# Kernel tuning notes

Measured on AMD Instinct MI355X. Metric: run time of the kernel, lower is better.

Reference implementation:

```python
import jax, jax.numpy as jnp
import numpy as np

EPS = 1e-5

def silu(x):
    return x * jax.nn.sigmoid(x)

def layernorm(x, g, b):
    m = jnp.mean(x, axis=-1, keepdims=True)
    v = jnp.var(x, axis=-1, keepdims=True)
    return (x - m) * jax.lax.rsqrt(v + EPS) * g + b

def mamba(x, in_w, conv_w, conv_b, xproj_w, dt_w, dt_b, A_log, Dp, out_w):
    # x: (B, L, d_model)
    B_, L, _ = x.shape
    d_inner, d_conv = conv_w.shape
    d_state = A_log.shape[1]
    dt_rank = dt_w.shape[1]
    xz = x @ in_w.T                     # (B, L, 2*d_inner)
    u, z = jnp.split(xz, 2, axis=-1)
    # causal depthwise conv1d, kernel size d_conv, truncated to L
    up = jnp.pad(u, ((0, 0), (d_conv - 1, 0), (0, 0))).transpose(0, 2, 1)  # (B, C, L+K-1)
    uc = jax.lax.conv_general_dilated(up, conv_w[:, None, :], (1,), 'VALID',
                                      feature_group_count=d_inner)        # (B, C, L)
    u = silu(uc.transpose(0, 2, 1) + conv_b)                               # (B, L, d_inner)
    dbc = u @ xproj_w.T                                                    # (B, L, dt_rank+2*d_state)
    dt, Bm, Cm = jnp.split(dbc, [dt_rank, dt_rank + d_state], axis=-1)
    delta = jax.nn.softplus(dt @ dt_w.T + dt_b)                            # (B, L, d_inner)
    A = -jnp.exp(A_log)                                                    # (d_inner, d_state)
    dA = jnp.exp(delta[..., None] * A)                                     # (B, L, d_inner, d_state)
    dBu = delta[..., None] * Bm[:, :, None, :] * u[..., None]

    def step(h, inp):
        dA_t, dBu_t, C_t = inp
        h = dA_t * h + dBu_t                                               # (B, d_inner, d_state)
        y = jnp.einsum('bdn,bn->bd', h, C_t)
        return h, y

    h0 = jnp.zeros((B_, d_inner, d_state), x.dtype)
    _, ys = jax.lax.scan(step, h0, (dA.transpose(1, 0, 2, 3),
                                    dBu.transpose(1, 0, 2, 3),
                                    Cm.transpose(1, 0, 2)))
    y = ys.transpose(1, 0, 2) + u * Dp
    y = y * silu(z)
    return y @ out_w.T

def decoder_layer(x,
                  f_in_w, f_conv_w, f_conv_b, f_xproj_w, f_dt_w, f_dt_b, f_A_log, f_D, f_out_w,
                  r_in_w, r_conv_w, r_conv_b, r_xproj_w, r_dt_w, r_dt_b, r_A_log, r_D, r_out_w,
                  conv1_w, conv1_b, conv2_w, conv2_b, ln1_g, ln1_b, ln2_g, ln2_b):
    fwd = mamba(x, f_in_w, f_conv_w, f_conv_b, f_xproj_w, f_dt_w, f_dt_b, f_A_log, f_D, f_out_w)
    bwd = jnp.flip(mamba(jnp.flip(x, axis=1), r_in_w, r_conv_w, r_conv_b, r_xproj_w,
                         r_dt_w, r_dt_b, r_A_log, r_D, r_out_w), axis=1)
    x1 = layernorm(x + fwd + bwd, ln1_g, ln1_b)
    # kernel-size-1 Conv1d == pointwise linear; dropout is identity at eval
    y = jax.nn.gelu(x1 @ conv1_w.T + conv1_b, approximate=False)
    y = y @ conv2_w.T + conv2_b
    return layernorm(x1 + y, ln2_g, ln2_b)

def setup_inputs() -> dict:
    key = jax.random.key(0)
    ks = jax.random.split(key, 32)
    d_model, d_state, d_inner, dt_rank, d_ff = 512, 16, 1024, 32, 2048
    B, L = 8, 512
    s = 0.02
    inp = {}
    inp['x'] = jax.random.normal(ks[0], (B, L, d_model), jnp.float32)
    i = 1
    for p in ('f', 'r'):
        inp[p + '_in_w'] = jax.random.normal(ks[i], (2 * d_inner, d_model)) * s; i += 1
        inp[p + '_conv_w'] = jax.random.normal(ks[i], (d_inner, 4)) * 0.2; i += 1
        inp[p + '_conv_b'] = jax.random.normal(ks[i], (d_inner,)) * s; i += 1
        inp[p + '_xproj_w'] = jax.random.normal(ks[i], (dt_rank + 2 * d_state, d_inner)) * s; i += 1
        inp[p + '_dt_w'] = jax.random.normal(ks[i], (d_inner, dt_rank)) * s; i += 1
        inp[p + '_dt_b'] = jax.random.normal(ks[i], (d_inner,)) * s; i += 1
        inp[p + '_A_log'] = jax.random.uniform(ks[i], (d_inner, d_state)); i += 1
        inp[p + '_D'] = jax.random.normal(ks[i], (d_inner,)) * s + 1.0; i += 1
        inp[p + '_out_w'] = jax.random.normal(ks[i], (d_model, d_inner)) * s; i += 1
    inp['conv1_w'] = jax.random.normal(ks[i], (d_ff, d_model)) * s; i += 1
    inp['conv1_b'] = jax.random.normal(ks[i], (d_ff,)) * s; i += 1
    inp['conv2_w'] = jax.random.normal(ks[i], (d_model, d_ff)) * s; i += 1
    inp['conv2_b'] = jax.random.normal(ks[i], (d_model,)) * s; i += 1
    inp['ln1_g'] = jnp.ones((d_model,)); inp['ln1_b'] = jnp.zeros((d_model,))
    inp['ln2_g'] = jnp.ones((d_model,)); inp['ln2_b'] = jnp.zeros((d_model,))
    return inp

def reference(x,
              f_in_w, f_conv_w, f_conv_b, f_xproj_w, f_dt_w, f_dt_b, f_A_log, f_D, f_out_w,
              r_in_w, r_conv_w, r_conv_b, r_xproj_w, r_dt_w, r_dt_b, r_A_log, r_D, r_out_w,
              conv1_w, conv1_b, conv2_w, conv2_b, ln1_g, ln1_b, ln2_g, ln2_b):
    return decoder_layer(x,
                         f_in_w, f_conv_w, f_conv_b, f_xproj_w, f_dt_w, f_dt_b, f_A_log, f_D, f_out_w,
                         r_in_w, r_conv_w, r_conv_b, r_xproj_w, r_dt_w, r_dt_b, r_A_log, r_D, r_out_w,
                         conv1_w, conv1_b, conv2_w, conv2_b, ln1_g, ln1_b, ln2_g, ln2_b)
```

## Files before the change

kernel.cpp:

```cpp
#include <hip/hip_runtime.h>
#include <hip/hip_bf16.h>

#define DEVINL __device__ __forceinline__

typedef short bf16x8 __attribute__((ext_vector_type(8)));
typedef float f32x4 __attribute__((ext_vector_type(4)));
typedef ushort ushort8v __attribute__((ext_vector_type(8)));

static constexpr int Bn = 8, Ln = 512, DM = 512, DI = 1024, DS = 16, DFF = 2048;
static constexpr int Mtok = Bn * Ln;
static constexpr int NCH = 32, CLS = 16;

DEVINL float bf2f(ushort u) { union { uint i; float f; } v; v.i = uint(u) << 16; return v.f; }
DEVINL ushort f2bf(float f) {
  union { float f; uint i; } v; v.f = f;
  uint r = v.i + 0x7FFF + ((v.i >> 16) & 1);
  return ushort(r >> 16);
}

#define GLOAD16(gp, lp)                                                        \
  __builtin_amdgcn_global_load_lds(                                            \
      (const __attribute__((address_space(1))) void*)(gp),                     \
      (__attribute__((address_space(3))) void*)(lp), 16, 0, 0)

struct CvtJob { const float* src; ushort* dst; int blk0; int _pad; };
struct CvtTab { CvtJob j[11]; };

__global__ __launch_bounds__(256)
void cvt_k(CvtTab tb, int njobs) {
  const int blk = blockIdx.x;
  int ji = 0;
#pragma unroll
  for (int k = 1; k < 11; ++k)
    if (k < njobs && tb.j[k].blk0 <= blk) ji = k;
  const CvtJob J = tb.j[ji];
  const size_t base = (size_t)(blk - J.blk0) * 2048 + (size_t)threadIdx.x * 8;
  float4 a = *(const float4*)(J.src + base);
  float4 b = *(const float4*)(J.src + base + 4);
  ushort8v o;
  o[0] = f2bf(a.x); o[1] = f2bf(a.y); o[2] = f2bf(a.z); o[3] = f2bf(a.w);
  o[4] = f2bf(b.x); o[5] = f2bf(b.y); o[6] = f2bf(b.z); o[7] = f2bf(b.w);
  *(ushort8v*)(J.dst + base) = o;
}

template<int BM, int BN, int WM, int WN, int EPI, int OUTF32, int DUALK>
__global__ __launch_bounds__(256)
void gemm_lds(const ushort* __restrict__ A0, const ushort* __restrict__ W0,
              void* __restrict__ C0v, const float* __restrict__ bias0,
              const ushort* __restrict__ A1, const ushort* __restrict__ W1,
              void* __restrict__ C1v, const float* __restrict__ bias1,
              const ushort* __restrict__ Ab0, const ushort* __restrict__ Wb0,
              int K, int lda, int ldw, int ldc, int Kb, int ldab, int ldwb)
{
  constexpr int MT = BM / WM / 16, NT = BN / WN / 16;
  constexpr int RA = BM * 32 / 2048, RB = BN * 32 / 2048;
  __shared__ ushort As[BM * 32];
  __shared__ ushort Bs[BN * 32];

  const ushort* Ap = blockIdx.z ? A1 : A0;
  const ushort* Wp = blockIdx.z ? W1 : W0;
  void* Cv         = blockIdx.z ? C1v : C0v;
  const float* bia = blockIdx.z ? bias1 : bias0;

  const int tid = threadIdx.x, lane = tid & 63, wv = tid >> 6;
  const int wm = wv / WN, wn = wv % WN;
  const int mbase = blockIdx.x * BM, nbase = blockIdx.y * BN;
  const int r = lane & 15, ko = (lane >> 4) * 8;

  f32x4 acc[MT][NT];
#pragma unroll
  for (int mi = 0; mi < MT; ++mi)
#pragma unroll
    for (int ni = 0; ni < NT; ++ni) acc[mi][ni] = (f32x4){0.f, 0.f, 0.f, 0.f};

  for (int blkK = 0; blkK < (DUALK ? 2 : 1); ++blkK) {
    const ushort* Au = (DUALK && blkK) ? Ab0 : Ap;
    const ushort* Wu = (DUALK && blkK) ? Wb0 : Wp;
    const int Ku  = (DUALK && blkK) ? Kb : K;
    const int ldau = (DUALK && blkK) ? ldab : lda;
    const int ldwu = (DUALK && blkK) ? ldwb : ldw;

    for (int k0 = 0; k0 < Ku; k0 += 32) {
      __syncthreads();
#pragma unroll
      for (int i = 0; i < RA; ++i) {
        const int e = i * 2048 + wv * 512 + lane * 8;
        const int row = e >> 5, ck = e & 31;
        GLOAD16(Au + (size_t)(mbase + row) * ldau + k0 + ck,
                (ushort*)As + i * 2048 + wv * 512);
      }
#pragma unroll
      for (int i = 0; i < RB; ++i) {
        const int e = i * 2048 + wv * 512 + lane * 8;
        const int row = e >> 5, ck = e & 31;
        GLOAD16(Wu + (size_t)(nbase + row) * ldwu + k0 + ck,
                (ushort*)Bs + i * 2048 + wv * 512);
      }
      __syncthreads();

      bf16x8 af[MT], bfv[NT];
#pragma unroll
      for (int mi = 0; mi < MT; ++mi)
        af[mi] = *(const bf16x8*)&As[(wm * MT * 16 + mi * 16 + r) * 32 + ko];
#pragma unroll
      for (int ni = 0; ni < NT; ++ni)
        bfv[ni] = *(const bf16x8*)&Bs[(wn * NT * 16 + ni * 16 + r) * 32 + ko];
#pragma unroll
      for (int mi = 0; mi < MT; ++mi)
#pragma unroll
        for (int ni = 0; ni < NT; ++ni)
          acc[mi][ni] = __builtin_amdgcn_mfma_f32_16x16x32_bf16(af[mi], bfv[ni], acc[mi][ni], 0, 0, 0);
    }
  }

  const int rr = (lane >> 4) * 4, cc = lane & 15;
#pragma unroll
  for (int ni = 0; ni < NT; ++ni) {
    const int col = nbase + wn * NT * 16 + ni * 16 + cc;
    float bsv = 0.f;
    if (EPI >= 1) bsv = bia[col];
#pragma unroll
    for (int mi = 0; mi < MT; ++mi) {
#pragma unroll
      for (int j = 0; j < 4; ++j) {
        const int row = mbase + wm * MT * 16 + mi * 16 + rr + j;
        float v = acc[mi][ni][j] + bsv;
        if (EPI == 2) v = (v > 20.f) ? v : __logf(1.f + __expf(v));
        if (EPI == 3) v = 0.5f * v * (1.f + erff(v * 0.70710678f));
        if (OUTF32) ((float*)Cv)[(size_t)row * ldc + col] = v;
        else        ((ushort*)Cv)[(size_t)row * ldc + col] = f2bf(v);
      }
    }
  }
}

template<int WAVES_M, int WAVES_N, int MT, int NT, int EPI, int OUTF32>
__global__ __launch_bounds__(WAVES_M * WAVES_N * 64)
void gemm_k(const ushort* __restrict__ A0, const ushort* __restrict__ W0,
            void* __restrict__ C0v, const float* __restrict__ bias0,
            const ushort* __restrict__ A1, const ushort* __restrict__ W1,
            void* __restrict__ C1v, const float* __restrict__ bias1,
            int K, int lda, int ldw, int ldc)
{
  const ushort* A   = blockIdx.z ? A1 : A0;
  const ushort* W   = blockIdx.z ? W1 : W0;
  void* Cv          = blockIdx.z ? C1v : C0v;
  const float* bia  = blockIdx.z ? bias1 : bias0;

  const int tid = threadIdx.x, lane = tid & 63, wv = tid >> 6;
  const int wm = wv / WAVES_N, wn = wv % WAVES_N;
  const int r = lane & 15, ko = (lane >> 4) * 8;
  const int mbase = blockIdx.x * (WAVES_M * MT * 16) + wm * (MT * 16);
  const int nbase = blockIdx.y * (WAVES_N * NT * 16) + wn * (NT * 16);

  f32x4 acc[MT][NT];
#pragma unroll
  for (int mi = 0; mi < MT; ++mi)
#pragma unroll
    for (int ni = 0; ni < NT; ++ni) acc[mi][ni] = (f32x4){0.f, 0.f, 0.f, 0.f};

  const ushort* arow[MT];
  const ushort* wrow[NT];
#pragma unroll
  for (int mi = 0; mi < MT; ++mi) arow[mi] = A + (size_t)(mbase + mi * 16 + r) * lda + ko;
#pragma unroll
  for (int ni = 0; ni < NT; ++ni) wrow[ni] = W + (size_t)(nbase + ni * 16 + r) * ldw + ko;
  for (int k0 = 0; k0 < K; k0 += 32) {
    bf16x8 av[MT], bv[NT];
#pragma unroll
    for (int mi = 0; mi < MT; ++mi) av[mi] = *(const bf16x8*)(arow[mi] + k0);
#pragma unroll
    for (int ni = 0; ni < NT; ++ni) bv[ni] = *(const bf16x8*)(wrow[ni] + k0);
#pragma unroll
    for (int mi = 0; mi < MT; ++mi)
#pragma unroll
      for (int ni = 0; ni < NT; ++ni)
        acc[mi][ni] = __builtin_amdgcn_mfma_f32_16x16x32_bf16(av[mi], bv[ni], acc[mi][ni], 0, 0, 0);
  }

  const int rr = (lane >> 4) * 4, cc = lane & 15;
#pragma unroll
  for (int ni = 0; ni < NT; ++ni) {
    const int col = nbase + ni * 16 + cc;
    float bsv = 0.f;
    if (EPI >= 1) bsv = bia[col];
#pragma unroll
    for (int mi = 0; mi < MT; ++mi) {
#pragma unroll
      for (int j = 0; j < 4; ++j) {
        const int row = mbase + mi * 16 + rr + j;
        float v = acc[mi][ni][j] + bsv;
        if (EPI == 2) v = (v > 20.f) ? v : __logf(1.f + __expf(v));
        if (OUTF32) ((float*)Cv)[(size_t)row * ldc + col] = v;
        else        ((ushort*)Cv)[(size_t)row * ldc + col] = f2bf(v);
      }
    }
  }
}

__global__ __launch_bounds__(256)
void xproj_k(const ushort* __restrict__ A0, const ushort* __restrict__ W0,
             ushort* __restrict__ C0,
             const ushort* __restrict__ A1, const ushort* __restrict__ W1,
             ushort* __restrict__ C1)
{
  const ushort* A = blockIdx.z ? A1 : A0;
  const ushort* W = blockIdx.z ? W1 : W0;
  ushort* C       = blockIdx.z ? C1 : C0;

  const int tid = threadIdx.x, lane = tid & 63, wv = tid >> 6;
  const int r = lane & 15, ko = (lane >> 4) * 8;
  const int mbase = blockIdx.x * 16;
  const int nbase = wv * 16;

  f32x4 acc = (f32x4){0.f, 0.f, 0.f, 0.f};
  const ushort* ap = A + (size_t)(mbase + r) * DI + ko;
  const ushort* wp = W + (size_t)(nbase + r) * DI + ko;
#pragma unroll 4
  for (int k0 = 0; k0 < DI; k0 += 32) {
    const bf16x8 av = *(const bf16x8*)(ap + k0);
    const bf16x8 bv = *(const bf16x8*)(wp + k0);
    acc = __builtin_amdgcn_mfma_f32_16x16x32_bf16(av, bv, acc, 0, 0, 0);
  }
  const int cc = lane & 15, rr = (lane >> 4) * 4;
#pragma unroll
  for (int j = 0; j < 4; ++j)
    C[(size_t)(mbase + rr + j) * 64 + nbase + cc] = f2bf(acc[j]);
}

__global__ __launch_bounds__(256)
void conv_k(const ushort* __restrict__ xz_f, const ushort* __restrict__ xz_r,
            const float* __restrict__ fw, const float* __restrict__ fb,
            const float* __restrict__ rw, const float* __restrict__ rb,
            ushort* __restrict__ u_f, ushort* __restrict__ u_r,
            ushort* __restrict__ gz_f, ushort* __restrict__ gz_r)
{
  int idx = blockIdx.x * 256 + threadIdx.x;
  int dir = idx >> 19;
  int rem = idx & ((1 << 19) - 1);
  int bt = rem >> 7;
  int c0 = (rem & 127) * 8;
  int b = bt >> 9, t = bt & 511;
  const ushort* xz = dir ? xz_r : xz_f;
  const float* cw = dir ? rw : fw;
  const float* cb = dir ? rb : fb;
  ushort* uo = dir ? u_r : u_f;
  ushort* go = dir ? gz_r : gz_f;

  float acc[8];
#pragma unroll
  for (int j = 0; j < 8; ++j) acc[j] = cb[c0 + j];
  float wgt[8][4];
#pragma unroll
  for (int j = 0; j < 8; ++j) {
    float4 w4 = *(const float4*)(cw + (size_t)(c0 + j) * 4);
    wgt[j][0] = w4.x; wgt[j][1] = w4.y; wgt[j][2] = w4.z; wgt[j][3] = w4.w;
  }
#pragma unroll
  for (int k = 0; k < 4; ++k) {
    int tt = dir ? (t + 3 - k) : (t - 3 + k);
    if (tt < 0 || tt >= Ln) continue;
    ushort8v v = *(const ushort8v*)(xz + ((size_t)(b * Ln + tt) * 2048 + c0));
#pragma unroll
    for (int j = 0; j < 8; ++j) acc[j] += wgt[j][k] * bf2f(v[j]);
  }
  ushort8v outv;
#pragma unroll
  for (int j = 0; j < 8; ++j) {
    float s = acc[j];
    outv[j] = f2bf(s / (1.f + __expf(-s)));
  }
  *(ushort8v*)(uo + (size_t)bt * DI + c0) = outv;

  ushort8v zv = *(const ushort8v*)(xz + ((size_t)bt * 2048 + DI + c0));
  ushort8v gv;
#pragma unroll
  for (int j = 0; j < 8; ++j) {
    float z = bf2f(zv[j]);
    gv[j] = f2bf(z / (1.f + __expf(-z)));
  }
  *(ushort8v*)(go + (size_t)bt * DI + c0) = gv;
}

__global__ __launch_bounds__(256, 4)
void scan1_k(const ushort* __restrict__ delta_f, const ushort* __restrict__ delta_r,
             const ushort* __restrict__ u_f, const ushort* __restrict__ u_r,
             const ushort* __restrict__ dbc_f, const ushort* __restrict__ dbc_r,
             const float* __restrict__ fA, const float* __restrict__ rA,
             float4* __restrict__ hloc, float* __restrict__ Sa)
{
  const int bid = blockIdx.x;
  const int part = bid & 3, chunk = (bid >> 2) & 31, b = (bid >> 7) & 7, dir = bid >> 10;
  const int tid = threadIdx.x, c = part * 256 + tid;

  const ushort* dl_p = dir ? delta_r : delta_f;
  const ushort* u_p  = dir ? u_r : u_f;
  const ushort* dbc  = dir ? dbc_r : dbc_f;
  const float*  Alog = dir ? rA : fA;

  __shared__ float Bs[CLS][16];
  {
    const int s = tid >> 4, n = tid & 15;
    const int t = dir ? (Ln - 1 - (chunk * CLS + s)) : (chunk * CLS + s);
    Bs[s][n] = bf2f(dbc[(size_t)(b * Ln + t) * 64 + 32 + n]);
  }
  __syncthreads();

  float a2[16];
  {
    const float4* Ar = (const float4*)(Alog + (size_t)c * 16);
#pragma unroll
    for (int g = 0; g < 4; ++g) {
      float4 av = Ar[g];
      a2[g*4+0] = -__expf(av.x) * 1.44269504f;
      a2[g*4+1] = -__expf(av.y) * 1.44269504f;
      a2[g*4+2] = -__expf(av.z) * 1.44269504f;
      a2[g*4+3] = -__expf(av.w) * 1.44269504f;
    }
  }

  const int t0 = dir ? (Ln - 1 - chunk * CLS) : (chunk * CLS);
  const int stp = (dir ? -1 : 1) * DI;
  const ushort* dlp = dl_p + (size_t)(b * Ln + t0) * DI + c;
  const ushort* up  = u_p  + (size_t)(b * Ln + t0) * DI + c;

  float h[16];
#pragma unroll
  for (int n = 0; n < 16; ++n) h[n] = 0.f;
  float S = 0.f;

#pragma unroll 2
  for (int s = 0; s < CLS; ++s) {
    const float dl = bf2f(*dlp); dlp += stp;
    const float uv = bf2f(*up); up += stp;
    const float du = dl * uv;
    S += dl;
#pragma unroll
    for (int g = 0; g < 4; ++g) {
      const float4 Bv = ((const float4*)Bs[s])[g];
      h[g*4+0] = fmaf(exp2f(dl * a2[g*4+0]), h[g*4+0], du * Bv.x);
      h[g*4+1] = fmaf(exp2f(dl * a2[g*4+1]), h[g*4+1], du * Bv.y);
      h[g*4+2] = fmaf(exp2f(dl * a2[g*4+2]), h[g*4+2], du * Bv.z);
      h[g*4+3] = fmaf(exp2f(dl * a2[g*4+3]), h[g*4+3], du * Bv.w);
    }
  }
  const size_t o = ((size_t)((dir * 8 + b) * NCH + chunk) * 1024 + c);
#pragma unroll
  for (int g = 0; g < 4; ++g)
    hloc[o * 4 + g] = (float4){h[g*4+0], h[g*4+1], h[g*4+2], h[g*4+3]};
  Sa[o] = S;
}

__global__ __launch_bounds__(256, 4)
void scan2_k(float4* __restrict__ hloc, const float* __restrict__ Sa,
             const float* __restrict__ fA, const float* __restrict__ rA)
{
  const int idx = blockIdx.x * 256 + threadIdx.x;
  const int ng = idx & 3, c = (idx >> 2) & 1023, b = (idx >> 12) & 7, dir = idx >> 15;
  const float* Alog = dir ? rA : fA;
  float a2[4];
  {
    const float4 av = *(const float4*)(Alog + (size_t)c * 16 + ng * 4);
    a2[0] = -__expf(av.x) * 1.44269504f;
    a2[1] = -__expf(av.y) * 1.44269504f;
    a2[2] = -__expf(av.z) * 1.44269504f;
    a2[3] = -__expf(av.w) * 1.44269504f;
  }
  float4 h = (float4){0.f, 0.f, 0.f, 0.f};
  const size_t base = (size_t)(dir * 8 + b) * NCH * 1024 + c;
#pragma unroll
  for (int k = 0; k < NCH; ++k) {
    const size_t o = base + (size_t)k * 1024;
    const float S = Sa[o];
    const float4 hl = hloc[o * 4 + ng];
    hloc[o * 4 + ng] = h;
    h.x = fmaf(exp2f(a2[0] * S), h.x, hl.x);
    h.y = fmaf(exp2f(a2[1] * S), h.y, hl.y);
    h.z = fmaf(exp2f(a2[2] * S), h.z, hl.z);
    h.w = fmaf(exp2f(a2[3] * S), h.w, hl.w);
  }
}

__global__ __launch_bounds__(256, 4)
void scan3_k(const ushort* __restrict__ delta_f, const ushort* __restrict__ delta_r,
             const ushort* __restrict__ u_f, const ushort* __restrict__ u_r,
             const ushort* __restrict__ dbc_f, const ushort* __restrict__ dbc_r,
             const ushort* __restrict__ gz_f, const ushort* __restrict__ gz_r,
             const float* __restrict__ fA, const float* __restrict__ fD,
             const float* __restrict__ rA, const float* __restrict__ rD,
             const float4* __restrict__ hin,
             ushort* __restrict__ ym_f, ushort* __restrict__ ym_r)
{
  const int bid = blockIdx.x;
  const int part = bid & 3, chunk = (bid >> 2) & 31, b = (bid >> 7) & 7, dir = bid >> 10;
  const int tid = threadIdx.x, c = part * 256 + tid;

  const ushort* dl_p = dir ? delta_r : delta_f;
  const ushort* u_p  = dir ? u_r : u_f;
  const ushort* dbc  = dir ? dbc_r : dbc_f;
  const ushort* gz   = dir ? gz_r : gz_f;
  const float*  Alog = dir ? rA : fA;
  const float*  Dw   = dir ? rD : fD;
  ushort* ym         = dir ? ym_r : ym_f;

  __shared__ float Bs[CLS][16], Cs[CLS][16];
  {
    const int s = tid >> 5, k = tid & 31;
#pragma unroll
    for (int p = 0; p < 2; ++p) {
      const int ss = s + p * 8;
      const int t = dir ? (Ln - 1 - (chunk * CLS + ss)) : (chunk * CLS + ss);
      const float val = bf2f(dbc[(size_t)(b * Ln + t) * 64 + 32 + k]);
      if (k < 16) Bs[ss][k] = val; else Cs[ss][k - 16] = val;
    }
  }
  __syncthreads();

  float a2[16];
  {
    const float4* Ar = (const float4*)(Alog + (size_t)c * 16);
#pragma unroll
    for (int g = 0; g < 4; ++g) {
      float4 av = Ar[g];
      a2[g*4+0] = -__expf(av.x) * 1.44269504f;
      a2[g*4+1] = -__expf(av.y) * 1.44269504f;
      a2[g*4+2] = -__expf(av.z) * 1.44269504f;
      a2[g*4+3] = -__expf(av.w) * 1.44269504f;
    }
  }
  const float Dc = Dw[c];

  float h[16];
  {
    const size_t o = ((size_t)((dir * 8 + b) * NCH + chunk) * 1024 + c) * 4;
#pragma unroll
    for (int g = 0; g < 4; ++g) {
      const float4 hv = hin[o + g];
      h[g*4+0] = hv.x; h[g*4+1] = hv.y; h[g*4+2] = hv.z; h[g*4+3] = hv.w;
    }
  }

  const int t0 = dir ? (Ln - 1 - chunk * CLS) : (chunk * CLS);
  const int stp = (dir ? -1 : 1) * DI;
  const ushort* dlp = dl_p + (size_t)(b * Ln + t0) * DI + c;
  const ushort* up  = u_p  + (size_t)(b * Ln + t0) * DI + c;
  const ushort* gp  = gz   + (size_t)(b * Ln + t0) * DI + c;
  ushort*       ymp = ym   + (size_t)(b * Ln + t0) * DI + c;

#pragma unroll 2
  for (int s = 0; s < CLS; ++s) {
    const float dl = bf2f(*dlp); dlp += stp;
    const float uv = bf2f(*up); up += stp;
    const float gg = bf2f(*gp); gp += stp;
    const float du = dl * uv;
    float y = 0.f;
#pragma unroll
    for (int g = 0; g < 4; ++g) {
      const float4 Bv = ((const float4*)Bs[s])[g];
      const float4 Cw = ((const float4*)Cs[s])[g];
      h[g*4+0] = fmaf(exp2f(dl * a2[g*4+0]), h[g*4+0], du * Bv.x); y = fmaf(h[g*4+0], Cw.x, y);
      h[g*4+1] = fmaf(exp2f(dl * a2[g*4+1]), h[g*4+1], du * Bv.y); y = fmaf(h[g*4+1], Cw.y, y);
      h[g*4+2] = fmaf(exp2f(dl * a2[g*4+2]), h[g*4+2], du * Bv.z); y = fmaf(h[g*4+2], Cw.z, y);
      h[g*4+3] = fmaf(exp2f(dl * a2[g*4+3]), h[g*4+3], du * Bv.w); y = fmaf(h[g*4+3], Cw.w, y);
    }
    *ymp = f2bf((y + uv * Dc) * gg); ymp += stp;
  }
}

template<int OUTF32>
__global__ __launch_bounds__(256)
void ln_k(const ushort* __restrict__ a, const ushort* __restrict__ b,
          const float* __restrict__ g, const float* __restrict__ bb,
          void* __restrict__ outv)
{
  const int row = blockIdx.x, tid = threadIdx.x;
  const size_t base = (size_t)row * DM;
  float v0 = bf2f(a[base + tid]) + bf2f(b[base + tid]);
  float v1 = bf2f(a[base + tid + 256]) + bf2f(b[base + tid + 256]);
  float s1 = v0 + v1, s2 = v0 * v0 + v1 * v1;
  for (int o = 32; o; o >>= 1) { s1 += __shfl_down(s1, o); s2 += __shfl_down(s2, o); }
  __shared__ float l1[4], l2[4];
  const int wv = tid >> 6, ln = tid & 63;
  if (ln == 0) { l1[wv] = s1; l2[wv] = s2; }
  __syncthreads();
  const float t1 = l1[0] + l1[1] + l1[2] + l1[3];
  const float t2 = l2[0] + l2[1] + l2[2] + l2[3];
  const float mean = t1 * (1.f / 512.f);
  const float var = t2 * (1.f / 512.f) - mean * mean;
  const float rs = rsqrtf(var + 1e-5f);
  const float o0 = (v0 - mean) * rs * g[tid] + bb[tid];
  const float o1 = (v1 - mean) * rs * g[tid + 256] + bb[tid + 256];
  if (OUTF32) {
    ((float*)outv)[base + tid] = o0;
    ((float*)outv)[base + tid + 256] = o1;
  } else {
    ((ushort*)outv)[base + tid] = f2bf(o0);
    ((ushort*)outv)[base + tid + 256] = f2bf(o1);
  }
}

extern "C" void kernel_launch(void* const* d_in, const int* in_sizes, int n_in,
                              void* d_out, int out_size, void* d_ws, size_t ws_size,
                              hipStream_t stream)
{
  const float* x        = (const float*)d_in[0];
  const float* f_in_w   = (const float*)d_in[1];
  const float* f_conv_w = (const float*)d_in[2];
  const float* f_conv_b = (const float*)d_in[3];
  const float* f_xproj  = (const float*)d_in[4];
  const float* f_dt_w   = (const float*)d_in[5];
  const float* f_dt_b   = (const float*)d_in[6];
  const float* f_A_log  = (const float*)d_in[7];
  const float* f_D      = (const float*)d_in[8];
  const float* f_out_w  = (const float*)d_in[9];
  const float* r_in_w   = (const float*)d_in[10];
  const float* r_conv_w = (const float*)d_in[11];
  const float* r_conv_b = (const float*)d_in[12];
  const float* r_xproj  = (const float*)d_in[13];
  const float* r_dt_w   = (const float*)d_in[14];
  const float* r_dt_b   = (const float*)d_in[15];
  const float* r_A_log  = (const float*)d_in[16];
  const float* r_D      = (const float*)d_in[17];
  const float* r_out_w  = (const float*)d_in[18];
  const float* conv1_w  = (const float*)d_in[19];
  const float* conv1_b  = (const float*)d_in[20];
  const float* conv2_w  = (const float*)d_in[21];
  const float* conv2_b  = (const float*)d_in[22];
  const float* ln1_g    = (const float*)d_in[23];
  const float* ln1_b    = (const float*)d_in[24];
  const float* ln2_g    = (const float*)d_in[25];
  const float* ln2_b    = (const float*)d_in[26];

  char* ws = (char*)d_ws;
  size_t off = 0;
  auto alloc = [&](size_t bytes) -> void* {
    void* p = ws + off;
    off += (bytes + 255) & ~(size_t)255;
    return p;
  };
  ushort* x_b     = (ushort*)alloc((size_t)Mtok * DM * 2);
  ushort* f_inw_b = (ushort*)alloc((size_t)2 * DI * DM * 2);
  ushort* r_inw_b = (ushort*)alloc((size_t)2 * DI * DM * 2);
  ushort* f_xp_b  = (ushort*)alloc((size_t)64 * DI * 2);
  ushort* r_xp_b  = (ushort*)alloc((size_t)64 * DI * 2);
  ushort* f_dtw_b = (ushort*)alloc((size_t)DI * 32 * 2);
  ushort* r_dtw_b = (ushort*)alloc((size_t)DI * 32 * 2);
  ushort* f_ow_b  = (ushort*)alloc((size_t)DM * DI * 2);
  ushort* r_ow_b  = (ushort*)alloc((size_t)DM * DI * 2);
  ushort* c1w_b   = (ushort*)alloc((size_t)DFF * DM * 2);
  ushort* c2w_b   = (ushort*)alloc((size_t)DM * DFF * 2);
  ushort* xz_f    = (ushort*)alloc((size_t)Mtok * 2048 * 2);
  ushort* xz_r    = (ushort*)alloc((size_t)Mtok * 2048 * 2);
  ushort* u_f     = (ushort*)alloc((size_t)Mtok * DI * 2);
  ushort* u_r     = (ushort*)alloc((size_t)Mtok * DI * 2);
  ushort* gz_f    = (ushort*)alloc((size_t)Mtok * DI * 2);
  ushort* gz_r    = (ushort*)alloc((size_t)Mtok * DI * 2);
  ushort* dbc_f   = (ushort*)alloc((size_t)Mtok * 64 * 2);
  ushort* dbc_r   = (ushort*)alloc((size_t)Mtok * 64 * 2);
  ushort* delta_f = (ushort*)alloc((size_t)Mtok * DI * 2);
  ushort* delta_r = (ushort*)alloc((size_t)Mtok * DI * 2);
  ushort* ym_f    = (ushort*)alloc((size_t)Mtok * DI * 2);
  ushort* ym_r    = (ushort*)alloc((size_t)Mtok * DI * 2);
  ushort* mo      = (ushort*)alloc((size_t)Mtok * DM * 2);
  ushort* x1      = (ushort*)alloc((size_t)Mtok * DM * 2);
  ushort* h1b     = (ushort*)alloc((size_t)Mtok * DFF * 2);
  ushort* y2      = (ushort*)alloc((size_t)Mtok * DM * 2);
  float4* hloc    = (float4*)alloc((size_t)2 * 8 * NCH * 1024 * 4 * 16);
  float*  Sa      = (float*)alloc((size_t)2 * 8 * NCH * 1024 * 4);
  (void)ws_size; (void)in_sizes; (void)n_in; (void)out_size;

  {
    CvtTab tb;
    int blk = 0, ji = 0;
    auto add = [&](const float* s, ushort* d, int n) {
      tb.j[ji].src = s; tb.j[ji].dst = d; tb.j[ji].blk0 = blk; tb.j[ji]._pad = 0;
      blk += n / 2048; ++ji;
    };
    add(x,       x_b,     Mtok * DM);
    add(f_in_w,  f_inw_b, 2 * DI * DM);
    add(r_in_w,  r_inw_b, 2 * DI * DM);
    add(f_xproj, f_xp_b,  64 * DI);
    add(r_xproj, r_xp_b,  64 * DI);
    add(f_dt_w,  f_dtw_b, DI * 32);
    add(r_dt_w,  r_dtw_b, DI * 32);
    add(f_out_w, f_ow_b,  DM * DI);
    add(r_out_w, r_ow_b,  DM * DI);
    add(conv1_w, c1w_b,   DFF * DM);
    add(conv2_w, c2w_b,   DM * DFF);
    cvt_k<<<dim3(blk), 256, 0, stream>>>(tb, ji);
  }

  gemm_lds<128, 128, 2, 2, 0, 0, 0><<<dim3(32, 16, 2), 256, 0, stream>>>(
      x_b, f_inw_b, xz_f, nullptr, x_b, r_inw_b, xz_r, nullptr,
      nullptr, nullptr, DM, DM, DM, 2048, 0, 0, 0);

  conv_k<<<dim3(2 * Mtok * DI / 8 / 256), 256, 0, stream>>>(
      xz_f, xz_r, f_conv_w, f_conv_b, r_conv_w, r_conv_b, u_f, u_r, gz_f, gz_r);

  xproj_k<<<dim3(256, 1, 2), 256, 0, stream>>>(
      u_f, f_xp_b, dbc_f, u_r, r_xp_b, dbc_r);

  gemm_k<4, 1, 1, 4, 2, 0><<<dim3(64, 16, 2), 256, 0, stream>>>(
      dbc_f, f_dtw_b, delta_f, f_dt_b, dbc_r, r_dtw_b, delta_r, r_dt_b,
      32, 64, 32, DI);

  scan1_k<<<dim3(2048), 256, 0, stream>>>(
      delta_f, delta_r, u_f, u_r, dbc_f, dbc_r, f_A_log, r_A_log, hloc, Sa);
  scan2_k<<<dim3(256), 256, 0, stream>>>(hloc, Sa, f_A_log, r_A_log);
  scan3_k<<<dim3(2048), 256, 0, stream>>>(
      delta_f, delta_r, u_f, u_r, dbc_f, dbc_r, gz_f, gz_r,
      f_A_log, f_D, r_A_log, r_D, hloc, ym_f, ym_r);

  gemm_lds<64, 64, 2, 2, 0, 0, 1><<<dim3(64, 8, 1), 256, 0, stream>>>(
      ym_f, f_ow_b, mo, nullptr, nullptr, nullptr, nullptr, nullptr,
      ym_r, r_ow_b, DI, DI, DI, DM, DI, DI, DI);

  ln_k<0><<<dim3(Mtok), 256, 0, stream>>>(x_b, mo, ln1_g, ln1_b, x1);

  gemm_lds<128, 128, 2, 2, 3, 0, 0><<<dim3(32, 16, 1), 256, 0, stream>>>(
      x1, c1w_b, h1b, conv1_b, nullptr, nullptr, nullptr, nullptr,
      nullptr, nullptr, DM, DM, DM, DFF, 0, 0, 0);

  gemm_lds<64, 64, 2, 2, 1, 0, 0><<<dim3(64, 8, 1), 256, 0, stream>>>(
      h1b, c2w_b, y2, conv2_b, nullptr, nullptr, nullptr, nullptr,
      nullptr, nullptr, DFF, DFF, DFF, DM, 0, 0, 0);

  ln_k<1><<<dim3(Mtok), 256, 0, stream>>>(x1, y2, ln2_g, ln2_b, (float*)d_out);
}
```

Before: 278.8 us.

## Split SSM state across thread pairs in scan kernels and relayout hloc

Each channel's 16-state recurrence is now handled by two adjacent threads with 8 states each, doubling the block count for scan1 and scan3. The y partial sums are combined with a lane shuffle and only one lane writes the output. The hloc buffer is relaid out as state-group-major so scan1, scan2 and scan3 access it with coalesced float4 loads and stores. The aim is more parallelism and lower register pressure in the chunked scan, at the cost of duplicated delta/u/gate loads per channel and a shuffle per timestep.

```diff
diff --git a/kernel.cpp b/kernel.cpp
--- a/kernel.cpp
+++ b/kernel.cpp
@@ -290,8 +290,9 @@
              float4* __restrict__ hloc, float* __restrict__ Sa)
 {
   const int bid = blockIdx.x;
-  const int part = bid & 3, chunk = (bid >> 2) & 31, b = (bid >> 7) & 7, dir = bid >> 10;
-  const int tid = threadIdx.x, c = part * 256 + tid;
+  const int part = bid & 7, chunk = (bid >> 3) & 31, b = (bid >> 8) & 7, dir = bid >> 11;
+  const int tid = threadIdx.x, half = tid & 1, c = part * 128 + (tid >> 1);
+  const int bd = dir * 8 + b;
 
   const ushort* dl_p = dir ? delta_r : delta_f;
   const ushort* u_p  = dir ? u_r : u_f;
@@ -306,11 +307,11 @@
   }
   __syncthreads();
 
-  float a2[16];
+  float a2[8];
   {
-    const float4* Ar = (const float4*)(Alog + (size_t)c * 16);
-#pragma unroll
-    for (int g = 0; g < 4; ++g) {
+    const float4* Ar = (const float4*)(Alog + (size_t)c * 16 + half * 8);
+#pragma unroll
+    for (int g = 0; g < 2; ++g) {
       float4 av = Ar[g];
       a2[g*4+0] = -__expf(av.x) * 1.44269504f;
       a2[g*4+1] = -__expf(av.y) * 1.44269504f;
@@ -324,9 +325,9 @@
   const ushort* dlp = dl_p + (size_t)(b * Ln + t0) * DI + c;
   const ushort* up  = u_p  + (size_t)(b * Ln + t0) * DI + c;
 
-  float h[16];
-#pragma unroll
-  for (int n = 0; n < 16; ++n) h[n] = 0.f;
+  float h[8];
+#pragma unroll
+  for (int n = 0; n < 8; ++n) h[n] = 0.f;
   float S = 0.f;
 
 #pragma unroll 2
@@ -336,19 +337,21 @@
     const float du = dl * uv;
     S += dl;
 #pragma unroll
-    for (int g = 0; g < 4; ++g) {
-      const float4 Bv = ((const float4*)Bs[s])[g];
+    for (int g = 0; g < 2; ++g) {
+      const float4 Bv = ((const float4*)Bs[s])[half * 2 + g];
       h[g*4+0] = fmaf(exp2f(dl * a2[g*4+0]), h[g*4+0], du * Bv.x);
       h[g*4+1] = fmaf(exp2f(dl * a2[g*4+1]), h[g*4+1], du * Bv.y);
       h[g*4+2] = fmaf(exp2f(dl * a2[g*4+2]), h[g*4+2], du * Bv.z);
       h[g*4+3] = fmaf(exp2f(dl * a2[g*4+3]), h[g*4+3], du * Bv.w);
     }
   }
-  const size_t o = ((size_t)((dir * 8 + b) * NCH + chunk) * 1024 + c);
-#pragma unroll
-  for (int g = 0; g < 4; ++g)
-    hloc[o * 4 + g] = (float4){h[g*4+0], h[g*4+1], h[g*4+2], h[g*4+3]};
-  Sa[o] = S;
+#pragma unroll
+  for (int g = 0; g < 2; ++g) {
+    const size_t o = ((size_t)(half * 2 + g) * 16 * NCH + (size_t)bd * NCH + chunk) * 1024 + c;
+    hloc[o] = (float4){h[g*4+0], h[g*4+1], h[g*4+2], h[g*4+3]};
+  }
+  if (half == 0)
+    Sa[((size_t)bd * NCH + chunk) * 1024 + c] = S;
 }
 
 __global__ __launch_bounds__(256, 4)
@@ -357,6 +360,7 @@
 {
   const int idx = blockIdx.x * 256 + threadIdx.x;
   const int ng = idx & 3, c = (idx >> 2) & 1023, b = (idx >> 12) & 7, dir = idx >> 15;
+  const int bd = dir * 8 + b;
   const float* Alog = dir ? rA : fA;
   float a2[4];
   {
@@ -367,13 +371,12 @@
     a2[3] = -__expf(av.w) * 1.44269504f;
   }
   float4 h = (float4){0.f, 0.f, 0.f, 0.f};
-  const size_t base = (size_t)(dir * 8 + b) * NCH * 1024 + c;
 #pragma unroll
   for (int k = 0; k < NCH; ++k) {
-    const size_t o = base + (size_t)k * 1024;
-    const float S = Sa[o];
-    const float4 hl = hloc[o * 4 + ng];
-    hloc[o * 4 + ng] = h;
+    const size_t o = ((size_t)ng * 16 * NCH + (size_t)bd * NCH + k) * 1024 + c;
+    const float S = Sa[((size_t)bd * NCH + k) * 1024 + c];
+    const float4 hl = hloc[o];
+    hloc[o] = h;
     h.x = fmaf(exp2f(a2[0] * S), h.x, hl.x);
     h.y = fmaf(exp2f(a2[1] * S), h.y, hl.y);
     h.z = fmaf(exp2f(a2[2] * S), h.z, hl.z);
@@ -392,8 +395,9 @@
              ushort* __restrict__ ym_f, ushort* __restrict__ ym_r)
 {
   const int bid = blockIdx.x;
-  const int part = bid & 3, chunk = (bid >> 2) & 31, b = (bid >> 7) & 7, dir = bid >> 10;
-  const int tid = threadIdx.x, c = part * 256 + tid;
+  const int part = bid & 7, chunk = (bid >> 3) & 31, b = (bid >> 8) & 7, dir = bid >> 11;
+  const int tid = threadIdx.x, half = tid & 1, c = part * 128 + (tid >> 1);
+  const int bd = dir * 8 + b;
 
   const ushort* dl_p = dir ? delta_r : delta_f;
   const ushort* u_p  = dir ? u_r : u_f;
@@ -416,11 +420,11 @@
   }
   __syncthreads();
 
-  float a2[16];
+  float a2[8];
   {
-    const float4* Ar = (const float4*)(Alog + (size_t)c * 16);
-#pragma unroll
-    for (int g = 0; g < 4; ++g) {
+    const float4* Ar = (const float4*)(Alog + (size_t)c * 16 + half * 8);
+#pragma unroll
+    for (int g = 0; g < 2; ++g) {
       float4 av = Ar[g];
       a2[g*4+0] = -__expf(av.x) * 1.44269504f;
       a2[g*4+1] = -__expf(av.y) * 1.44269504f;
@@ -430,14 +434,12 @@
   }
   const float Dc = Dw[c];
 
-  float h[16];
-  {
-    const size_t o = ((size_t)((dir * 8 + b) * NCH + chunk) * 1024 + c) * 4;
-#pragma unroll
-    for (int g = 0; g < 4; ++g) {
-      const float4 hv = hin[o + g];
-      h[g*4+0] = hv.x; h[g*4+1] = hv.y; h[g*4+2] = hv.z; h[g*4+3] = hv.w;
-    }
+  float h[8];
+#pragma unroll
+  for (int g = 0; g < 2; ++g) {
+    const size_t o = ((size_t)(half * 2 + g) * 16 * NCH + (size_t)bd * NCH + chunk) * 1024 + c;
+    const float4 hv = hin[o];
+    h[g*4+0] = hv.x; h[g*4+1] = hv.y; h[g*4+2] = hv.z; h[g*4+3] = hv.w;
   }
 
   const int t0 = dir ? (Ln - 1 - chunk * CLS) : (chunk * CLS);
@@ -455,15 +457,18 @@
     const float du = dl * uv;
     float y = 0.f;
 #pragma unroll
-    for (int g = 0; g < 4; ++g) {
-      const float4 Bv = ((const float4*)Bs[s])[g];
-      const float4 Cw = ((const float4*)Cs[s])[g];
+    for (int g = 0; g < 2; ++g) {
+      const float4 Bv = ((const float4*)Bs[s])[half * 2 + g];
+      const float4 Cw = ((const float4*)Cs[s])[half * 2 + g];
       h[g*4+0] = fmaf(exp2f(dl * a2[g*4+0]), h[g*4+0], du * Bv.x); y = fmaf(h[g*4+0], Cw.x, y);
       h[g*4+1] = fmaf(exp2f(dl * a2[g*4+1]), h[g*4+1], du * Bv.y); y = fmaf(h[g*4+1], Cw.y, y);
       h[g*4+2] = fmaf(exp2f(dl * a2[g*4+2]), h[g*4+2], du * Bv.z); y = fmaf(h[g*4+2], Cw.z, y);
       h[g*4+3] = fmaf(exp2f(dl * a2[g*4+3]), h[g*4+3], du * Bv.w); y = fmaf(h[g*4+3], Cw.w, y);
     }
-    *ymp = f2bf((y + uv * Dc) * gg); ymp += stp;
+    y += __shfl_xor(y, 1);
+    if (half == 0)
+      *ymp = f2bf((y + uv * Dc) * gg);
+    ymp += stp;
   }
 }
 
@@ -565,8 +570,8 @@
   ushort* x1      = (ushort*)alloc((size_t)Mtok * DM * 2);
   ushort* h1b     = (ushort*)alloc((size_t)Mtok * DFF * 2);
   ushort* y2      = (ushort*)alloc((size_t)Mtok * DM * 2);
-  float4* hloc    = (float4*)alloc((size_t)2 * 8 * NCH * 1024 * 4 * 16);
-  float*  Sa      = (float*)alloc((size_t)2 * 8 * NCH * 1024 * 4);
+  float4* hloc    = (float4*)alloc((size_t)4 * 16 * NCH * 1024 * 16);
+  float*  Sa      = (float*)alloc((size_t)16 * NCH * 1024 * 4);
   (void)ws_size; (void)in_sizes; (void)n_in; (void)out_size;
 
   {
@@ -604,10 +609,10 @@
       dbc_f, f_dtw_b, delta_f, f_dt_b, dbc_r, r_dtw_b, delta_r, r_dt_b,
       32, 64, 32, DI);
 
-  scan1_k<<<dim3(2048), 256, 0, stream>>>(
+  scan1_k<<<dim3(4096), 256, 0, stream>>>(
       delta_f, delta_r, u_f, u_r, dbc_f, dbc_r, f_A_log, r_A_log, hloc, Sa);
   scan2_k<<<dim3(256), 256, 0, stream>>>(hloc, Sa, f_A_log, r_A_log);
-  scan3_k<<<dim3(2048), 256, 0, stream>>>(
+  scan3_k<<<dim3(4096), 256, 0, stream>>>(
       delta_f, delta_r, u_f, u_r, dbc_f, dbc_r, gz_f, gz_r,
       f_A_log, f_D, r_A_log, r_D, hloc, ym_f, ym_r);
 
```

Result: slower. 285.6 us (+2.5%).

## Move scan decay coefficients to LDS and make chunk-state buffers group-major

Applied to the files above, without the earlier changes.

In scan1 and scan3 the per-channel decay coefficients a2 now live in a transposed shared-memory array instead of sixteen registers, which lowers register pressure and may raise occupancy. The cost is an LDS read on every step of the recurrence. The chunk-state buffer hloc is re-laid out so the four float4 state groups are outermost. Consecutive threads (consecutive channels) then read and write consecutive float4s, giving coalesced accesses in scan1, scan2 and scan3.

```diff
diff --git a/kernel.cpp b/kernel.cpp
--- a/kernel.cpp
+++ b/kernel.cpp
@@ -292,6 +292,7 @@
   const int bid = blockIdx.x;
   const int part = bid & 3, chunk = (bid >> 2) & 31, b = (bid >> 7) & 7, dir = bid >> 10;
   const int tid = threadIdx.x, c = part * 256 + tid;
+  const int bd = dir * 8 + b;
 
   const ushort* dl_p = dir ? delta_r : delta_f;
   const ushort* u_p  = dir ? u_r : u_f;
@@ -299,25 +300,24 @@
   const float*  Alog = dir ? rA : fA;
 
   __shared__ float Bs[CLS][16];
+  __shared__ float a2T[16][256];
   {
     const int s = tid >> 4, n = tid & 15;
     const int t = dir ? (Ln - 1 - (chunk * CLS + s)) : (chunk * CLS + s);
     Bs[s][n] = bf2f(dbc[(size_t)(b * Ln + t) * 64 + 32 + n]);
   }
-  __syncthreads();
-
-  float a2[16];
   {
     const float4* Ar = (const float4*)(Alog + (size_t)c * 16);
 #pragma unroll
     for (int g = 0; g < 4; ++g) {
       float4 av = Ar[g];
-      a2[g*4+0] = -__expf(av.x) * 1.44269504f;
-      a2[g*4+1] = -__expf(av.y) * 1.44269504f;
-      a2[g*4+2] = -__expf(av.z) * 1.44269504f;
-      a2[g*4+3] = -__expf(av.w) * 1.44269504f;
-    }
-  }
+      a2T[g*4+0][tid] = -__expf(av.x) * 1.44269504f;
+      a2T[g*4+1][tid] = -__expf(av.y) * 1.44269504f;
+      a2T[g*4+2][tid] = -__expf(av.z) * 1.44269504f;
+      a2T[g*4+3][tid] = -__expf(av.w) * 1.44269504f;
+    }
+  }
+  __syncthreads();
 
   const int t0 = dir ? (Ln - 1 - chunk * CLS) : (chunk * CLS);
   const int stp = (dir ? -1 : 1) * DI;
@@ -338,17 +338,18 @@
 #pragma unroll
     for (int g = 0; g < 4; ++g) {
       const float4 Bv = ((const float4*)Bs[s])[g];
-      h[g*4+0] = fmaf(exp2f(dl * a2[g*4+0]), h[g*4+0], du * Bv.x);
-      h[g*4+1] = fmaf(exp2f(dl * a2[g*4+1]), h[g*4+1], du * Bv.y);
-      h[g*4+2] = fmaf(exp2f(dl * a2[g*4+2]), h[g*4+2], du * Bv.z);
-      h[g*4+3] = fmaf(exp2f(dl * a2[g*4+3]), h[g*4+3], du * Bv.w);
-    }
-  }
-  const size_t o = ((size_t)((dir * 8 + b) * NCH + chunk) * 1024 + c);
-#pragma unroll
-  for (int g = 0; g < 4; ++g)
-    hloc[o * 4 + g] = (float4){h[g*4+0], h[g*4+1], h[g*4+2], h[g*4+3]};
-  Sa[o] = S;
+      h[g*4+0] = fmaf(exp2f(dl * a2T[g*4+0][tid]), h[g*4+0], du * Bv.x);
+      h[g*4+1] = fmaf(exp2f(dl * a2T[g*4+1][tid]), h[g*4+1], du * Bv.y);
+      h[g*4+2] = fmaf(exp2f(dl * a2T[g*4+2][tid]), h[g*4+2], du * Bv.z);
+      h[g*4+3] = fmaf(exp2f(dl * a2T[g*4+3][tid]), h[g*4+3], du * Bv.w);
+    }
+  }
+#pragma unroll
+  for (int g = 0; g < 4; ++g) {
+    const size_t o = ((size_t)g * 16 * NCH + (size_t)bd * NCH + chunk) * 1024 + c;
+    hloc[o] = (float4){h[g*4+0], h[g*4+1], h[g*4+2], h[g*4+3]};
+  }
+  Sa[((size_t)bd * NCH + chunk) * 1024 + c] = S;
 }
 
 __global__ __launch_bounds__(256, 4)
@@ -357,6 +358,7 @@
 {
   const int idx = blockIdx.x * 256 + threadIdx.x;
   const int ng = idx & 3, c = (idx >> 2) & 1023, b = (idx >> 12) & 7, dir = idx >> 15;
+  const int bd = dir * 8 + b;
   const float* Alog = dir ? rA : fA;
   float a2[4];
   {
@@ -367,13 +369,12 @@
     a2[3] = -__expf(av.w) * 1.44269504f;
   }
   float4 h = (float4){0.f, 0.f, 0.f, 0.f};
-  const size_t base = (size_t)(dir * 8 + b) * NCH * 1024 + c;
 #pragma unroll
   for (int k = 0; k < NCH; ++k) {
-    const size_t o = base + (size_t)k * 1024;
-    const float S = Sa[o];
-    const float4 hl = hloc[o * 4 + ng];
-    hloc[o * 4 + ng] = h;
+    const size_t o = ((size_t)ng * 16 * NCH + (size_t)bd * NCH + k) * 1024 + c;
+    const float S = Sa[((size_t)bd * NCH + k) * 1024 + c];
+    const float4 hl = hloc[o];
+    hloc[o] = h;
     h.x = fmaf(exp2f(a2[0] * S), h.x, hl.x);
     h.y = fmaf(exp2f(a2[1] * S), h.y, hl.y);
     h.z = fmaf(exp2f(a2[2] * S), h.z, hl.z);
@@ -394,6 +395,7 @@
   const int bid = blockIdx.x;
   const int part = bid & 3, chunk = (bid >> 2) & 31, b = (bid >> 7) & 7, dir = bid >> 10;
   const int tid = threadIdx.x, c = part * 256 + tid;
+  const int bd = dir * 8 + b;
 
   const ushort* dl_p = dir ? delta_r : delta_f;
   const ushort* u_p  = dir ? u_r : u_f;
@@ -404,6 +406,7 @@
   ushort* ym         = dir ? ym_r : ym_f;
 
   __shared__ float Bs[CLS][16], Cs[CLS][16];
+  __shared__ float a2T[16][256];
   {
     const int s = tid >> 5, k = tid & 31;
 #pragma unroll
@@ -414,30 +417,27 @@
       if (k < 16) Bs[ss][k] = val; else Cs[ss][k - 16] = val;
     }
   }
-  __syncthreads();
-
-  float a2[16];
   {
     const float4* Ar = (const float4*)(Alog + (size_t)c * 16);
 #pragma unroll
     for (int g = 0; g < 4; ++g) {
       float4 av = Ar[g];
-      a2[g*4+0] = -__expf(av.x) * 1.44269504f;
-      a2[g*4+1] = -__expf(av.y) * 1.44269504f;
-      a2[g*4+2] = -__expf(av.z) * 1.44269504f;
-      a2[g*4+3] = -__expf(av.w) * 1.44269504f;
-    }
-  }
+      a2T[g*4+0][tid] = -__expf(av.x) * 1.44269504f;
+      a2T[g*4+1][tid] = -__expf(av.y) * 1.44269504f;
+      a2T[g*4+2][tid] = -__expf(av.z) * 1.44269504f;
+      a2T[g*4+3][tid] = -__expf(av.w) * 1.44269504f;
+    }
+  }
+  __syncthreads();
+
   const float Dc = Dw[c];
 
   float h[16];
-  {
-    const size_t o = ((size_t)((dir * 8 + b) * NCH + chunk) * 1024 + c) * 4;
-#pragma unroll
-    for (int g = 0; g < 4; ++g) {
-      const float4 hv = hin[o + g];
-      h[g*4+0] = hv.x; h[g*4+1] = hv.y; h[g*4+2] = hv.z; h[g*4+3] = hv.w;
-    }
+#pragma unroll
+  for (int g = 0; g < 4; ++g) {
+    const size_t o = ((size_t)g * 16 * NCH + (size_t)bd * NCH + chunk) * 1024 + c;
+    const float4 hv = hin[o];
+    h[g*4+0] = hv.x; h[g*4+1] = hv.y; h[g*4+2] = hv.z; h[g*4+3] = hv.w;
   }
 
   const int t0 = dir ? (Ln - 1 - chunk * CLS) : (chunk * CLS);
@@ -458,10 +458,10 @@
     for (int g = 0; g < 4; ++g) {
       const float4 Bv = ((const float4*)Bs[s])[g];
       const float4 Cw = ((const float4*)Cs[s])[g];
-      h[g*4+0] = fmaf(exp2f(dl * a2[g*4+0]), h[g*4+0], du * Bv.x); y = fmaf(h[g*4+0], Cw.x, y);
-      h[g*4+1] = fmaf(exp2f(dl * a2[g*4+1]), h[g*4+1], du * Bv.y); y = fmaf(h[g*4+1], Cw.y, y);
-      h[g*4+2] = fmaf(exp2f(dl * a2[g*4+2]), h[g*4+2], du * Bv.z); y = fmaf(h[g*4+2], Cw.z, y);
-      h[g*4+3] = fmaf(exp2f(dl * a2[g*4+3]), h[g*4+3], du * Bv.w); y = fmaf(h[g*4+3], Cw.w, y);
+      h[g*4+0] = fmaf(exp2f(dl * a2T[g*4+0][tid]), h[g*4+0], du * Bv.x); y = fmaf(h[g*4+0], Cw.x, y);
+      h[g*4+1] = fmaf(exp2f(dl * a2T[g*4+1][tid]), h[g*4+1], du * Bv.y); y = fmaf(h[g*4+1], Cw.y, y);
+      h[g*4+2] = fmaf(exp2f(dl * a2T[g*4+2][tid]), h[g*4+2], du * Bv.z); y = fmaf(h[g*4+2], Cw.z, y);
+      h[g*4+3] = fmaf(exp2f(dl * a2T[g*4+3][tid]), h[g*4+3], du * Bv.w); y = fmaf(h[g*4+3], Cw.w, y);
     }
     *ymp = f2bf((y + uv * Dc) * gg); ymp += stp;
   }
@@ -565,8 +565,8 @@
   ushort* x1      = (ushort*)alloc((size_t)Mtok * DM * 2);
   ushort* h1b     = (ushort*)alloc((size_t)Mtok * DFF * 2);
   ushort* y2      = (ushort*)alloc((size_t)Mtok * DM * 2);
-  float4* hloc    = (float4*)alloc((size_t)2 * 8 * NCH * 1024 * 4 * 16);
-  float*  Sa      = (float*)alloc((size_t)2 * 8 * NCH * 1024 * 4);
+  float4* hloc    = (float4*)alloc((size_t)4 * 16 * NCH * 1024 * 16);
+  float*  Sa      = (float*)alloc((size_t)16 * NCH * 1024 * 4);
   (void)ws_size; (void)in_sizes; (void)n_in; (void)out_size;
 
   {
```

Measured after the change: 280.4 us. No clear change (+0.6%).
